# Performance work log

Measured on AMD Instinct MI355X. Metric: run time of the kernel, lower is better.

## Reference

```python
import jax, jax.numpy as jnp
import numpy as np

NUM_HEADS = 16
ROPE_BASE = 10000.0


def _rotate_half(x):
    d = x.shape[-1] // 2
    return jnp.concatenate([-x[..., d:], x[..., :d]], axis=-1)


def _rope_cos_sin(seq_len, rot_dim, dtype):
    # LlamaRotaryEmbedding(dim=rot_dim): inv_freq over even indices, emb = cat(freqs, freqs)
    inv_freq = 1.0 / (ROPE_BASE ** (jnp.arange(0, rot_dim, 2, dtype=jnp.float32) / rot_dim))
    t = jnp.arange(seq_len, dtype=jnp.float32)
    freqs = t[:, None] * inv_freq[None, :]            # [S, rot_dim/2]
    emb = jnp.concatenate([freqs, freqs], axis=-1)    # [S, rot_dim]
    return jnp.cos(emb).astype(dtype), jnp.sin(emb).astype(dtype)


def setup_inputs() -> dict:
    key = jax.random.key(0)
    ks = jax.random.split(key, 9)
    B, S, H = 2, 2048, 2048
    L = H // 8
    s = 0.02
    return {
        "hidden_states": jax.random.normal(ks[0], (B, S, H), jnp.float32),
        "Wkv_d": jax.random.normal(ks[1], (H, L), jnp.float32) * s,
        "Wq_d": jax.random.normal(ks[2], (H, L), jnp.float32) * s,
        "Wk_u": jax.random.normal(ks[3], (L, H // 2), jnp.float32) * s,
        "Wq_u": jax.random.normal(ks[4], (L, H // 2), jnp.float32) * s,
        "Wv_u": jax.random.normal(ks[5], (L, H), jnp.float32) * s,
        "Wrk": jax.random.normal(ks[6], (H, H // 2), jnp.float32) * s,
        "Wrq": jax.random.normal(ks[7], (L, H // 2), jnp.float32) * s,
        "Wo": jax.random.normal(ks[8], (H, H), jnp.float32) * s,
    }


def reference(hidden_states, Wkv_d, Wq_d, Wk_u, Wq_u, Wv_u, Wrk, Wrq, Wo):
    B, S, H = hidden_states.shape
    nh = NUM_HEADS
    hd = H // nh          # 128
    rd = hd // 2          # 64 (rope / content half width)

    kv_d = hidden_states @ Wkv_d            # [B,S,L]
    q_d = hidden_states @ Wq_d              # [B,S,L]

    k_c = (kv_d @ Wk_u).reshape(B, S, nh, rd)
    q_c = (q_d @ Wq_u).reshape(B, S, nh, rd)
    v = (kv_d @ Wv_u).reshape(B, S, nh, hd)
    k_r = (hidden_states @ Wrk).reshape(B, S, nh, rd)
    q_r = (q_d @ Wrq).reshape(B, S, nh, rd)

    cos, sin = _rope_cos_sin(S, rd, hidden_states.dtype)
    cos = cos[None, :, None, :]             # [1,S,1,rd] broadcast over batch/heads
    sin = sin[None, :, None, :]
    q_r = q_r * cos + _rotate_half(q_r) * sin
    k_r = k_r * cos + _rotate_half(k_r) * sin

    q = jnp.concatenate([q_c, q_r], axis=-1).transpose(0, 2, 1, 3)  # [B,nh,S,hd]
    k = jnp.concatenate([k_c, k_r], axis=-1).transpose(0, 2, 1, 3)
    v = v.transpose(0, 2, 1, 3)

    scale = jnp.asarray(hd, q.dtype) ** -0.5
    scores = jnp.einsum("bhqd,bhkd->bhqk", q, k) * scale
    causal = jnp.tril(jnp.ones((S, S), dtype=bool))
    scores = jnp.where(causal[None, None], scores, jnp.finfo(scores.dtype).min)
    attn = jax.nn.softmax(scores, axis=-1)
    y = jnp.einsum("bhqk,bhkd->bhqd", attn, v)
    y = y.transpose(0, 2, 1, 3).reshape(B, S, H)
    return y @ Wo
```

## Files before the change

### kernel.cpp

```cpp
#include <hip/hip_runtime.h>
#include <hip/hip_bf16.h>
#include <math.h>


typedef __attribute__((ext_vector_type(8))) short bf16x8;
typedef __attribute__((ext_vector_type(4))) float f32x4;
typedef unsigned int u32;

#define MFMA16(a, b, c) __builtin_amdgcn_mfma_f32_16x16x32_bf16(a, b, c, 0, 0, 0)

#define QSCALE_F (0.08838834764831845f * 1.4426950408889634f)
#define ROPE_EXP (-0.2878231366242557f)

__device__ __forceinline__ short f2bs(float f) {
  __hip_bfloat16 h = __float2bfloat16(f);
  return *reinterpret_cast<short*>(&h);
}
__device__ __forceinline__ float bs2f(short s) {
  union { unsigned int u; float f; } v;
  v.u = ((unsigned int)(unsigned short)s) << 16;
  return v.f;
}
__device__ __forceinline__ u32 fbits(float f) {
  union { float f; u32 u; } v; v.f = f; return v.u;
}

__device__ __forceinline__ void async16(const void* g, void* l) {
  __builtin_amdgcn_global_load_lds(
      (const __attribute__((address_space(1))) u32*)(unsigned long long)g,
      (__attribute__((address_space(3))) u32*)(unsigned int)(unsigned long long)l,
      16, 0, 0);
}
__device__ __forceinline__ void wait_vm0() {
  __builtin_amdgcn_s_waitcnt(0x0f70);
}

__device__ __forceinline__ void xcd_remap(int& bx, int& by) {
  const int id = blockIdx.y * gridDim.x + blockIdx.x;
  const int nyp = gridDim.y >> 3;
  const int xcd = id & 7, t = id >> 3;
  by = xcd * nyp + (t % nyp);
  bx = t / nyp;
}

__device__ __forceinline__ void wtrans_tile(const float* __restrict__ W,
                                            short* __restrict__ Wt, int K, int N,
                                            int bx, int by, int tid) {
  __shared__ float t[32][33];
  int k0 = by * 32, n0 = bx * 32;
#pragma unroll
  for (int i = 0; i < 4; ++i) {
    int idx = tid + i * 256;
    int r = idx >> 5, c = idx & 31;
    t[r][c] = W[(size_t)(k0 + r) * N + n0 + c];
  }
  __syncthreads();
#pragma unroll
  for (int i = 0; i < 4; ++i) {
    int idx = tid + i * 256;
    int r = idx >> 5, c = idx & 31;
    Wt[(size_t)(n0 + r) * K + k0 + c] = f2bs(t[c][r]);
  }
}

__global__ __launch_bounds__(256) void prep_all(
    const float* __restrict__ hs, const float* __restrict__ Wkvd,
    const float* __restrict__ Wqd, const float* __restrict__ Wku,
    const float* __restrict__ Wqu, const float* __restrict__ Wvu,
    const float* __restrict__ Wrk, const float* __restrict__ Wrq,
    const float* __restrict__ Wo, short* __restrict__ hs_b,
    short* __restrict__ W1t, short* __restrict__ W2t,
    short* __restrict__ W3t, short* __restrict__ Wo_t) {
  const int b = blockIdx.x, tid = threadIdx.x;
  if (b < 8192) {
    int i = (b * 256 + tid) * 4;
    float4 v = *(const float4*)(hs + i);
    short4 o;
    o.x = f2bs(v.x); o.y = f2bs(v.y); o.z = f2bs(v.z); o.w = f2bs(v.w);
    *(short4*)(hs_b + i) = o;
  } else if (b < 8704) {
    int l = b - 8192; wtrans_tile(Wkvd, W1t, 2048, 256, l & 7, l >> 3, tid);
  } else if (b < 9216) {
    int l = b - 8704; wtrans_tile(Wqd, W1t + 256 * 2048, 2048, 256, l & 7, l >> 3, tid);
  } else if (b < 11264) {
    int l = b - 9216; wtrans_tile(Wrk, W1t + 512 * 2048, 2048, 1024, l & 31, l >> 5, tid);
  } else if (b < 11520) {
    int l = b - 11264; wtrans_tile(Wku, W2t, 256, 1024, l & 31, l >> 5, tid);
  } else if (b < 12032) {
    int l = b - 11520; wtrans_tile(Wvu, W2t + 1024 * 256, 256, 2048, l & 63, l >> 6, tid);
  } else if (b < 12288) {
    int l = b - 12032; wtrans_tile(Wqu, W3t, 256, 1024, l & 31, l >> 5, tid);
  } else if (b < 12544) {
    int l = b - 12288; wtrans_tile(Wrq, W3t + 1024 * 256, 256, 1024, l & 31, l >> 5, tid);
  } else {
    int l = b - 12544; wtrans_tile(Wo, Wo_t, 2048, 2048, l & 63, l >> 6, tid);
  }
}

__device__ __forceinline__ void cstore(float v, float* p) { *p = v; }
__device__ __forceinline__ void cstore(float v, short* p) { *p = f2bs(v); }

template <typename CT>
__global__ __launch_bounds__(256) void gemm_bt(const short* __restrict__ A, int lda,
                                               const short* __restrict__ Bt, int ldb,
                                               CT* __restrict__ C, int ldc, int K) {
  __shared__ short As[128 * 64];
  __shared__ short Bs[128 * 64];
  const int tid = threadIdx.x;
  const int wave = tid >> 6, lane = tid & 63;
  const int quad = lane >> 4, l15 = lane & 15;
  const int wm = wave & 1, wn = wave >> 1;
  int bx, by; xcd_remap(bx, by);
  const int row0 = by * 128, col0 = bx * 128;
  const int sr = tid >> 3;
  const int sc = ((tid & 7) ^ (sr & 7)) * 8;
  const short* Ag = A + (size_t)(row0 + sr) * lda + sc;
  const short* Bg = Bt + (size_t)(col0 + sr) * ldb + sc;
  const int rk = l15 & 7;

  f32x4 acc[4][4];
#pragma unroll
  for (int i = 0; i < 4; ++i)
#pragma unroll
    for (int j = 0; j < 4; ++j) acc[i][j] = {0.f, 0.f, 0.f, 0.f};

  for (int k0 = 0; k0 < K; k0 += 64) {
    __syncthreads();
#pragma unroll
    for (int i = 0; i < 4; ++i) {
      async16(Ag + (size_t)(i * 32) * lda + k0, &As[i * 2048 + tid * 8]);
      async16(Bg + (size_t)(i * 32) * ldb + k0, &Bs[i * 2048 + tid * 8]);
    }
    wait_vm0();
    __syncthreads();
#pragma unroll
    for (int s = 0; s < 2; ++s) {
      bf16x8 af[4], bfr[4];
#pragma unroll
      for (int i = 0; i < 4; ++i) {
        af[i]  = *(const bf16x8*)&As[(wm * 64 + i * 16 + l15) * 64 +
                                     ((s * 4 + quad) ^ rk) * 8];
        bfr[i] = *(const bf16x8*)&Bs[(wn * 64 + i * 16 + l15) * 64 +
                                     ((s * 4 + quad) ^ rk) * 8];
      }
#pragma unroll
      for (int i = 0; i < 4; ++i)
#pragma unroll
        for (int j = 0; j < 4; ++j)
          acc[i][j] = MFMA16(af[i], bfr[j], acc[i][j]);
    }
  }
#pragma unroll
  for (int i = 0; i < 4; ++i)
#pragma unroll
    for (int j = 0; j < 4; ++j)
#pragma unroll
      for (int r = 0; r < 4; ++r) {
        int row = row0 + wm * 64 + i * 16 + quad * 4 + r;
        int col = col0 + wn * 64 + j * 16 + l15;
        cstore(acc[i][j][r], &C[(size_t)row * ldc + col]);
      }
}

__global__ __launch_bounds__(256) void gemm1k(const short* __restrict__ A,
                                              const short* __restrict__ Bt,
                                              short* __restrict__ C1,
                                              short* __restrict__ kf) {
  __shared__ short As[128 * 64];
  __shared__ short Bs[128 * 64];
  const int tid = threadIdx.x;
  const int wave = tid >> 6, lane = tid & 63;
  const int quad = lane >> 4, l15 = lane & 15;
  const int wm = wave & 1, wn = wave >> 1;
  int bx, by; xcd_remap(bx, by);
  const int row0 = by * 128, col0 = bx * 128;
  const int sr = tid >> 3;
  const int sc = ((tid & 7) ^ (sr & 7)) * 8;
  const short* Ag = A + (size_t)(row0 + sr) * 2048 + sc;
  const short* Bg = Bt + (size_t)(col0 + sr) * 2048 + sc;
  const int rk = l15 & 7;

  f32x4 acc[4][4];
#pragma unroll
  for (int i = 0; i < 4; ++i)
#pragma unroll
    for (int j = 0; j < 4; ++j) acc[i][j] = {0.f, 0.f, 0.f, 0.f};

  for (int k0 = 0; k0 < 2048; k0 += 64) {
    __syncthreads();
#pragma unroll
    for (int i = 0; i < 4; ++i) {
      async16(Ag + (size_t)(i * 32) * 2048 + k0, &As[i * 2048 + tid * 8]);
      async16(Bg + (size_t)(i * 32) * 2048 + k0, &Bs[i * 2048 + tid * 8]);
    }
    wait_vm0();
    __syncthreads();
#pragma unroll
    for (int s = 0; s < 2; ++s) {
      bf16x8 af[4], bfr[4];
#pragma unroll
      for (int i = 0; i < 4; ++i) {
        af[i]  = *(const bf16x8*)&As[(wm * 64 + i * 16 + l15) * 64 +
                                     ((s * 4 + quad) ^ rk) * 8];
        bfr[i] = *(const bf16x8*)&Bs[(wn * 64 + i * 16 + l15) * 64 +
                                     ((s * 4 + quad) ^ rk) * 8];
      }
#pragma unroll
      for (int i = 0; i < 4; ++i)
#pragma unroll
        for (int j = 0; j < 4; ++j)
          acc[i][j] = MFMA16(af[i], bfr[j], acc[i][j]);
    }
  }

  if (bx < 4) {
#pragma unroll
    for (int i = 0; i < 4; ++i)
#pragma unroll
      for (int jj = 0; jj < 4; ++jj)
#pragma unroll
        for (int r = 0; r < 4; ++r) {
          int row = row0 + wm * 64 + i * 16 + quad * 4 + r;
          int col = col0 + wn * 64 + jj * 16 + l15;
          C1[(size_t)row * 512 + col] = f2bs(acc[i][jj][r]);
        }
  } else {
    const int colb = (bx - 4) * 128 + wn * 64 + l15;
    const int h = colb >> 6;
    const float ef0 = __expf(ROPE_EXP * (float)l15);
    const float ef1 = __expf(ROPE_EXP * (float)(l15 + 16));
#pragma unroll
    for (int i = 0; i < 4; ++i)
#pragma unroll
      for (int r = 0; r < 4; ++r) {
        int row = row0 + wm * 64 + i * 16 + quad * 4 + r;
        int s = row & 2047, b = row >> 11;
        float fs = (float)s;
        float a0 = fs * ef0, a1 = fs * ef1;
        float c0 = __cosf(a0), s0 = __sinf(a0);
        float c1 = __cosf(a1), s1 = __sinf(a1);
        float o0 = acc[i][0][r] * c0 - acc[i][2][r] * s0;
        float o2 = acc[i][2][r] * c0 + acc[i][0][r] * s0;
        float o1 = acc[i][1][r] * c1 - acc[i][3][r] * s1;
        float o3 = acc[i][3][r] * c1 + acc[i][1][r] * s1;
        short* kp = kf + (((size_t)(b * 16 + h) * 2048 + s) * 128 + 64 + l15);
        kp[0]  = f2bs(o0);
        kp[16] = f2bs(o1);
        kp[32] = f2bs(o2);
        kp[48] = f2bs(o3);
      }
  }
}

__global__ __launch_bounds__(256) void gemm23(const short* __restrict__ C1,
                                              const short* __restrict__ W2t,
                                              short* __restrict__ qf,
                                              short* __restrict__ kf,
                                              short* __restrict__ vt) {
  __shared__ short As[128 * 64];
  __shared__ short Bs[128 * 64];
  const int tid = threadIdx.x;
  const int wave = tid >> 6, lane = tid & 63;
  const int quad = lane >> 4, l15 = lane & 15;
  const int wm = wave & 1, wn = wave >> 1;
  int bx, by; xcd_remap(bx, by);
  const short* A = bx < 24 ? C1 : C1 + 256;
  const int row0 = by * 128;
  const int sr = tid >> 3;
  const int sc = ((tid & 7) ^ (sr & 7)) * 8;
  const short* Ag = A + (size_t)(row0 + sr) * 512 + sc;
  const short* Bg = W2t + (size_t)(bx * 128 + sr) * 256 + sc;
  const int rk = l15 & 7;

  f32x4 acc[4][4];
#pragma unroll
  for (int i = 0; i < 4; ++i)
#pragma unroll
    for (int j = 0; j < 4; ++j) acc[i][j] = {0.f, 0.f, 0.f, 0.f};

  for (int k0 = 0; k0 < 256; k0 += 64) {
    __syncthreads();
#pragma unroll
    for (int i = 0; i < 4; ++i) {
      async16(Ag + (size_t)(i * 32) * 512 + k0, &As[i * 2048 + tid * 8]);
      async16(Bg + (size_t)(i * 32) * 256 + k0, &Bs[i * 2048 + tid * 8]);
    }
    wait_vm0();
    __syncthreads();
#pragma unroll
    for (int s = 0; s < 2; ++s) {
      bf16x8 af[4], bfr[4];
#pragma unroll
      for (int i = 0; i < 4; ++i) {
        af[i]  = *(const bf16x8*)&As[(wm * 64 + i * 16 + l15) * 64 +
                                     ((s * 4 + quad) ^ rk) * 8];
        bfr[i] = *(const bf16x8*)&Bs[(wn * 64 + i * 16 + l15) * 64 +
                                     ((s * 4 + quad) ^ rk) * 8];
      }
#pragma unroll
      for (int i = 0; i < 4; ++i)
#pragma unroll
        for (int j = 0; j < 4; ++j)
          acc[i][j] = MFMA16(af[i], bfr[j], acc[i][j]);
    }
  }

  if (bx < 8) {
    const int colb = bx * 128 + wn * 64 + l15;
    const int h = colb >> 6;
#pragma unroll
    for (int i = 0; i < 4; ++i)
#pragma unroll
      for (int r = 0; r < 4; ++r) {
        int row = row0 + wm * 64 + i * 16 + quad * 4 + r;
        int s = row & 2047, b = row >> 11;
        short* kp = kf + (((size_t)(b * 16 + h) * 2048 + s) * 128 + l15);
#pragma unroll
        for (int jj = 0; jj < 4; ++jj) kp[jj * 16] = f2bs(acc[i][jj][r]);
      }
  } else if (bx < 24) {
    const int b = row0 >> 11;
    const int s0 = row0 & 2047;
#pragma unroll
    for (int i = 0; i < 4; ++i)
#pragma unroll
      for (int jj = 0; jj < 4; ++jj) {
        int vcol = (bx - 8) * 128 + wn * 64 + jj * 16 + l15;
        int h = vcol >> 7, d = vcol & 127;
        int s = s0 + wm * 64 + i * 16 + quad * 4;
        short4 o;
        o.x = f2bs(acc[i][jj][0]); o.y = f2bs(acc[i][jj][1]);
        o.z = f2bs(acc[i][jj][2]); o.w = f2bs(acc[i][jj][3]);
        *(short4*)&vt[((size_t)((b * 16 + h) * 128 + d)) * 2048 + s] = o;
      }
  } else if (bx < 32) {
    const int colb = (bx - 24) * 128 + wn * 64 + l15;
    const int h = colb >> 6;
#pragma unroll
    for (int i = 0; i < 4; ++i)
#pragma unroll
      for (int r = 0; r < 4; ++r) {
        int row = row0 + wm * 64 + i * 16 + quad * 4 + r;
        int s = row & 2047, b = row >> 11;
        short* qp = qf + (((size_t)(b * 16 + h) * 2048 + s) * 128 + l15);
#pragma unroll
        for (int jj = 0; jj < 4; ++jj) qp[jj * 16] = f2bs(acc[i][jj][r] * QSCALE_F);
      }
  } else {
    const int colb = (bx - 32) * 128 + wn * 64 + l15;
    const int h = colb >> 6;
    const float ef0 = __expf(ROPE_EXP * (float)l15);
    const float ef1 = __expf(ROPE_EXP * (float)(l15 + 16));
#pragma unroll
    for (int i = 0; i < 4; ++i)
#pragma unroll
      for (int r = 0; r < 4; ++r) {
        int row = row0 + wm * 64 + i * 16 + quad * 4 + r;
        int s = row & 2047, b = row >> 11;
        float fs = (float)s;
        float a0 = fs * ef0, a1 = fs * ef1;
        float c0 = __cosf(a0), s0 = __sinf(a0);
        float c1 = __cosf(a1), s1 = __sinf(a1);
        float o0 = (acc[i][0][r] * c0 - acc[i][2][r] * s0) * QSCALE_F;
        float o2 = (acc[i][2][r] * c0 + acc[i][0][r] * s0) * QSCALE_F;
        float o1 = (acc[i][1][r] * c1 - acc[i][3][r] * s1) * QSCALE_F;
        float o3 = (acc[i][3][r] * c1 + acc[i][1][r] * s1) * QSCALE_F;
        short* qp = qf + (((size_t)(b * 16 + h) * 2048 + s) * 128 + 64 + l15);
        qp[0]  = f2bs(o0);
        qp[16] = f2bs(o1);
        qp[32] = f2bs(o2);
        qp[48] = f2bs(o3);
      }
  }
}

__global__ __launch_bounds__(256) void attn_split(const short* __restrict__ qf,
                                                  const short* __restrict__ kf,
                                                  const short* __restrict__ vt,
                                                  short* __restrict__ part,
                                                  float2* __restrict__ ml) {
  __shared__ short Ks[2][32 * 128];
  __shared__ short Vs[2][128 * 32];
  __shared__ short Pw[4][16 * 32];
  const int lid = blockIdx.x;
  const int bh = (lid & 7) * 4 + ((lid >> 3) & 3);
  const int x  = lid >> 5;
  const int tid = threadIdx.x;
  const int wave = tid >> 6, lane = tid & 63;
  const int quad = lane >> 4, l15 = lane & 15;
  const int krow_l = tid >> 4;
  const int kcol_sw = ((tid & 15) ^ krow_l) * 8;
  const int vrow_l = tid >> 2;
  const int vcol_sw = ((tid & 3) ^ (vrow_l & 3) ^ ((vrow_l >> 2) & 3)) * 8;
  const short* kgB = kf + (((size_t)bh * 2048) + krow_l) * 128 + kcol_sw;
  const short* vgB = vt + ((size_t)bh * 128 + vrow_l) * 2048 + vcol_sw;
  const int pswz = l15 & 6;

  for (int pass = 0; pass < 2; ++pass) {
    const int qt = pass ? 31 - x : x;
    const int ks = pass ? qt + 1 : 0;
    const int ke = pass ? 2 * (qt + 1) : x + 1;
    const int q0w = qt * 64 + wave * 16;

    bf16x8 qfr[4];
    {
      const short* qp = qf + (((size_t)bh * 2048) + q0w + l15) * 128;
#pragma unroll
      for (int kc = 0; kc < 4; ++kc)
        qfr[kc] = *(const bf16x8*)(qp + kc * 32 + quad * 8);
    }
    float m_i = -INFINITY;
    float l_i = 0.f;
    f32x4 O[8];
#pragma unroll
    for (int dt = 0; dt < 8; ++dt) O[dt] = {0.f, 0.f, 0.f, 0.f};

    {
      const short* kg = kgB + (size_t)ks * 32 * 128;
      const short* vg = vgB + ks * 32;
#pragma unroll
      for (int i = 0; i < 2; ++i) {
        async16(kg + (size_t)i * 16 * 128, &Ks[0][i * 2048 + tid * 8]);
        async16(vg + (size_t)i * 64 * 2048, &Vs[0][i * 2048 + tid * 8]);
      }
    }
    wait_vm0();
    __syncthreads();

    int cur = 0;
    for (int kt = ks; kt < ke; ++kt) {
      const int k0 = kt * 32;
      if (kt + 1 < ke) {
        const short* kg = kgB + (size_t)(kt + 1) * 32 * 128;
        const short* vg = vgB + (kt + 1) * 32;
#pragma unroll
        for (int i = 0; i < 2; ++i) {
          async16(kg + (size_t)i * 16 * 128, &Ks[cur ^ 1][i * 2048 + tid * 8]);
          async16(vg + (size_t)i * 64 * 2048, &Vs[cur ^ 1][i * 2048 + tid * 8]);
        }
      }

      f32x4 St[2];
#pragma unroll
      for (int j = 0; j < 2; ++j) St[j] = {0.f, 0.f, 0.f, 0.f};
      __builtin_amdgcn_s_setprio(1);
#pragma unroll
      for (int kc = 0; kc < 4; ++kc) {
        bf16x8 kb[2];
#pragma unroll
        for (int j = 0; j < 2; ++j)
          kb[j] = *(const bf16x8*)&Ks[cur][(j * 16 + l15) * 128 +
                                          (((kc * 4 + quad) ^ l15) & 15) * 8];
#pragma unroll
        for (int j = 0; j < 2; ++j)
          St[j] = MFMA16(kb[j], qfr[kc], St[j]);
      }
      __builtin_amdgcn_s_setprio(0);

      if (kt >= 2 * qt) {
#pragma unroll
        for (int j = 0; j < 2; ++j)
#pragma unroll
          for (int r = 0; r < 4; ++r)
            if (k0 + j * 16 + quad * 4 + r > q0w + l15)
              St[j][r] = -INFINITY;
      }

      {
        float mt = -INFINITY;
#pragma unroll
        for (int j = 0; j < 2; ++j)
#pragma unroll
          for (int r = 0; r < 4; ++r) mt = fmaxf(mt, St[j][r]);
        if (!__all(mt <= m_i + 8.f)) {
          mt = fmaxf(mt, __shfl_xor(mt, 16));
          mt = fmaxf(mt, __shfl_xor(mt, 32));
          float mnew = fmaxf(m_i, mt);
          float a = __builtin_amdgcn_exp2f(m_i - mnew);
          m_i = mnew;
          l_i *= a;
#pragma unroll
          for (int dt = 0; dt < 8; ++dt)
#pragma unroll
            for (int r = 0; r < 4; ++r) O[dt][r] *= a;
        }
        float ms = (m_i == -INFINITY) ? 0.f : m_i;
        float ps = 0.f;
#pragma unroll
        for (int j = 0; j < 2; ++j)
#pragma unroll
          for (int r = 0; r < 4; ++r) {
            float p = __builtin_amdgcn_exp2f(St[j][r] - ms);
            St[j][r] = p;
            ps += p;
          }
        l_i += ps;
      }

      {
        int pr = l15;
#pragma unroll
        for (int j = 0; j < 2; ++j) {
          u32 u0 = (fbits(St[j][1]) & 0xffff0000u) | (fbits(St[j][0]) >> 16);
          u32 u1 = (fbits(St[j][3]) & 0xffff0000u) | (fbits(St[j][2]) >> 16);
          uint2 pk; pk.x = u0; pk.y = u1;
          int g = (j * 4 + quad) ^ pswz;
          *(uint2*)&Pw[wave][pr * 32 + g * 4] = pk;
        }
      }

      __builtin_amdgcn_s_setprio(1);
      bf16x8 pa;
      {
        int g = (quad * 2) ^ pswz;
        pa = *(const bf16x8*)&Pw[wave][l15 * 32 + g * 4];
      }
#pragma unroll
      for (int dt = 0; dt < 8; ++dt) {
        bf16x8 vb = *(const bf16x8*)&Vs[cur][(dt * 16 + l15) * 32 +
                                            ((quad ^ (l15 & 3) ^ ((l15 >> 2) & 3)) & 3) * 8];
        O[dt] = MFMA16(vb, pa, O[dt]);
      }
      __builtin_amdgcn_s_setprio(0);

      wait_vm0();
      __syncthreads();
      cur ^= 1;
    }

    const int pidx = (bh * 32 + qt) * 2 + pass;
    short* pb = part + (size_t)pidx * 64 * 128;
    {
      int qrow = wave * 16 + l15;
#pragma unroll
      for (int dt = 0; dt < 8; ++dt) {
        short4 o;
        o.x = f2bs(O[dt][0]); o.y = f2bs(O[dt][1]);
        o.z = f2bs(O[dt][2]); o.w = f2bs(O[dt][3]);
        *(short4*)&pb[(size_t)qrow * 128 + dt * 16 + quad * 4] = o;
      }
    }
    float lr = l_i;
    lr += __shfl_xor(lr, 16);
    lr += __shfl_xor(lr, 32);
    if (quad == 0) {
      float2 v; v.x = m_i; v.y = lr;
      ml[pidx * 64 + wave * 16 + l15] = v;
    }
  }
}

__global__ __launch_bounds__(256) void attn_merge(const short* __restrict__ part,
                                                  const float2* __restrict__ ml,
                                                  short* __restrict__ y) {
  const int l = blockIdx.x;
  const int bh = ((l & 7) << 2) | ((l >> 3) & 3);
  const int qt = (l >> 5) & 31;
  const int b = bh >> 4, h = bh & 15;
  const int row = threadIdx.x >> 2, d0 = (threadIdx.x & 3) * 32;
  const int p1 = (bh * 32 + qt) * 2, p2 = p1 + 1;
  float2 a = ml[p1 * 64 + row], c = ml[p2 * 64 + row];
  float m = fmaxf(a.x, c.x);
  float a1 = __builtin_amdgcn_exp2f(a.x - m);
  float a2 = __builtin_amdgcn_exp2f(c.x - m);
  float invl = 1.f / (a.y * a1 + c.y * a2);
  a1 *= invl; a2 *= invl;
  const short* s1 = part + ((size_t)p1 * 64 + row) * 128 + d0;
  const short* s2 = part + ((size_t)p2 * 64 + row) * 128 + d0;
  short* yp = y + (((size_t)b * 2048 + qt * 64 + row) * 16 + h) * 128 + d0;
#pragma unroll
  for (int j = 0; j < 8; ++j) {
    short4 v1 = *(const short4*)(s1 + j * 4);
    short4 v2 = *(const short4*)(s2 + j * 4);
    short4 o;
    o.x = f2bs(bs2f(v1.x) * a1 + bs2f(v2.x) * a2);
    o.y = f2bs(bs2f(v1.y) * a1 + bs2f(v2.y) * a2);
    o.z = f2bs(bs2f(v1.z) * a1 + bs2f(v2.z) * a2);
    o.w = f2bs(bs2f(v1.w) * a1 + bs2f(v2.w) * a2);
    *(short4*)(yp + j * 4) = o;
  }
}

extern "C" void kernel_launch(void* const* d_in, const int* in_sizes, int n_in,
                              void* d_out, int out_size, void* d_ws, size_t ws_size,
                              hipStream_t stream) {
  const float* hs   = (const float*)d_in[0];
  const float* Wkvd = (const float*)d_in[1];
  const float* Wqd  = (const float*)d_in[2];
  const float* Wku  = (const float*)d_in[3];
  const float* Wqu  = (const float*)d_in[4];
  const float* Wvu  = (const float*)d_in[5];
  const float* Wrk  = (const float*)d_in[6];
  const float* Wrq  = (const float*)d_in[7];
  const float* Wo   = (const float*)d_in[8];
  float* out = (float*)d_out;
  char* ws = (char*)d_ws;
  const size_t MB = 1024ull * 1024ull;

  short* hs_b = (short*)(ws + 0 * MB);
  short* W1t  = (short*)(ws + 16 * MB);
  short* W2t  = (short*)(ws + 22 * MB);
  short* W3t  = W2t + 3072 * 256;
  short* C1   = (short*)(ws + 25 * MB);
  short* Wo_t = (short*)(ws + 77 * MB);
  short* q_f  = (short*)(ws + 85 * MB);
  short* k_f  = (short*)(ws + 101 * MB);
  short* v_t  = (short*)(ws + 117 * MB);
  short* y_b  = (short*)(ws + 133 * MB);
  short*  partb = (short*)(ws + 0 * MB);
  float2* mlb   = (float2*)(ws + 32 * MB);

  dim3 blk(256);
  prep_all<<<dim3(16640), blk, 0, stream>>>(hs, Wkvd, Wqd, Wku, Wqu, Wvu, Wrk,
                                            Wrq, Wo, hs_b, W1t, W2t, W3t, Wo_t);

  gemm1k<<<dim3(12, 32), blk, 0, stream>>>(hs_b, W1t, C1, k_f);
  gemm23<<<dim3(40, 32), blk, 0, stream>>>(C1, W2t, q_f, k_f, v_t);

  attn_split<<<dim3(1024), blk, 0, stream>>>(q_f, k_f, v_t, partb, mlb);
  attn_merge<<<dim3(1024), blk, 0, stream>>>(partb, mlb, y_b);

  gemm_bt<float><<<dim3(16, 32), blk, 0, stream>>>(y_b, 2048, Wo_t, 2048, out, 2048, 2048);
}
```

Measured before the change: 315.3 us.

## Double-buffer LDS tiles in GEMM kernels to overlap loads with MFMA

Converts the three projection GEMM kernels from single-buffered to double-buffered shared memory. The next K-tile is prefetched asynchronously while MFMAs run on the current one, and wave priority is raised during the compute phase. The goal is to hide global-load latency that the old load-wait-compute loop exposed every iteration. LDS use per block doubles to 64KB, which may lower occupancy.

Measured after the change: 289.4 us, median of 2. -8.2%, faster.

```diff
diff --git a/kernel.cpp b/kernel.cpp
--- a/kernel.cpp
+++ b/kernel.cpp
@@ -104,8 +104,8 @@
 __global__ __launch_bounds__(256) void gemm_bt(const short* __restrict__ A, int lda,
                                                const short* __restrict__ Bt, int ldb,
                                                CT* __restrict__ C, int ldc, int K) {
-  __shared__ short As[128 * 64];
-  __shared__ short Bs[128 * 64];
+  __shared__ short As[2][128 * 64];
+  __shared__ short Bs[2][128 * 64];
   const int tid = threadIdx.x;
   const int wave = tid >> 6, lane = tid & 63;
   const int quad = lane >> 4, l15 = lane & 15;
@@ -124,31 +124,44 @@
 #pragma unroll
     for (int j = 0; j < 4; ++j) acc[i][j] = {0.f, 0.f, 0.f, 0.f};
 
+#pragma unroll
+  for (int i = 0; i < 4; ++i) {
+    async16(Ag + (size_t)(i * 32) * lda, &As[0][i * 2048 + tid * 8]);
+    async16(Bg + (size_t)(i * 32) * ldb, &Bs[0][i * 2048 + tid * 8]);
+  }
+  wait_vm0();
+  __syncthreads();
+
+  int cur = 0;
   for (int k0 = 0; k0 < K; k0 += 64) {
-    __syncthreads();
-#pragma unroll
-    for (int i = 0; i < 4; ++i) {
-      async16(Ag + (size_t)(i * 32) * lda + k0, &As[i * 2048 + tid * 8]);
-      async16(Bg + (size_t)(i * 32) * ldb + k0, &Bs[i * 2048 + tid * 8]);
-    }
+    if (k0 + 64 < K) {
+#pragma unroll
+      for (int i = 0; i < 4; ++i) {
+        async16(Ag + (size_t)(i * 32) * lda + k0 + 64, &As[cur ^ 1][i * 2048 + tid * 8]);
+        async16(Bg + (size_t)(i * 32) * ldb + k0 + 64, &Bs[cur ^ 1][i * 2048 + tid * 8]);
+      }
+    }
+    __builtin_amdgcn_s_setprio(1);
+#pragma unroll
+    for (int s = 0; s < 2; ++s) {
+      bf16x8 af[4], bfr[4];
+#pragma unroll
+      for (int i = 0; i < 4; ++i) {
+        af[i]  = *(const bf16x8*)&As[cur][(wm * 64 + i * 16 + l15) * 64 +
+                                         ((s * 4 + quad) ^ rk) * 8];
+        bfr[i] = *(const bf16x8*)&Bs[cur][(wn * 64 + i * 16 + l15) * 64 +
+                                         ((s * 4 + quad) ^ rk) * 8];
+      }
+#pragma unroll
+      for (int i = 0; i < 4; ++i)
+#pragma unroll
+        for (int j = 0; j < 4; ++j)
+          acc[i][j] = MFMA16(af[i], bfr[j], acc[i][j]);
+    }
+    __builtin_amdgcn_s_setprio(0);
     wait_vm0();
     __syncthreads();
-#pragma unroll
-    for (int s = 0; s < 2; ++s) {
-      bf16x8 af[4], bfr[4];
-#pragma unroll
-      for (int i = 0; i < 4; ++i) {
-        af[i]  = *(const bf16x8*)&As[(wm * 64 + i * 16 + l15) * 64 +
-                                     ((s * 4 + quad) ^ rk) * 8];
-        bfr[i] = *(const bf16x8*)&Bs[(wn * 64 + i * 16 + l15) * 64 +
-                                     ((s * 4 + quad) ^ rk) * 8];
-      }
-#pragma unroll
-      for (int i = 0; i < 4; ++i)
-#pragma unroll
-        for (int j = 0; j < 4; ++j)
-          acc[i][j] = MFMA16(af[i], bfr[j], acc[i][j]);
-    }
+    cur ^= 1;
   }
 #pragma unroll
   for (int i = 0; i < 4; ++i)
@@ -166,8 +179,8 @@
                                               const short* __restrict__ Bt,
                                               short* __restrict__ C1,
                                               short* __restrict__ kf) {
-  __shared__ short As[128 * 64];
-  __shared__ short Bs[128 * 64];
+  __shared__ short As[2][128 * 64];
+  __shared__ short Bs[2][128 * 64];
   const int tid = threadIdx.x;
   const int wave = tid >> 6, lane = tid & 63;
   const int quad = lane >> 4, l15 = lane & 15;
@@ -186,31 +199,44 @@
 #pragma unroll
     for (int j = 0; j < 4; ++j) acc[i][j] = {0.f, 0.f, 0.f, 0.f};
 
+#pragma unroll
+  for (int i = 0; i < 4; ++i) {
+    async16(Ag + (size_t)(i * 32) * 2048, &As[0][i * 2048 + tid * 8]);
+    async16(Bg + (size_t)(i * 32) * 2048, &Bs[0][i * 2048 + tid * 8]);
+  }
+  wait_vm0();
+  __syncthreads();
+
+  int cur = 0;
   for (int k0 = 0; k0 < 2048; k0 += 64) {
-    __syncthreads();
-#pragma unroll
-    for (int i = 0; i < 4; ++i) {
-      async16(Ag + (size_t)(i * 32) * 2048 + k0, &As[i * 2048 + tid * 8]);
-      async16(Bg + (size_t)(i * 32) * 2048 + k0, &Bs[i * 2048 + tid * 8]);
-    }
+    if (k0 + 64 < 2048) {
+#pragma unroll
+      for (int i = 0; i < 4; ++i) {
+        async16(Ag + (size_t)(i * 32) * 2048 + k0 + 64, &As[cur ^ 1][i * 2048 + tid * 8]);
+        async16(Bg + (size_t)(i * 32) * 2048 + k0 + 64, &Bs[cur ^ 1][i * 2048 + tid * 8]);
+      }
+    }
+    __builtin_amdgcn_s_setprio(1);
+#pragma unroll
+    for (int s = 0; s < 2; ++s) {
+      bf16x8 af[4], bfr[4];
+#pragma unroll
+      for (int i = 0; i < 4; ++i) {
+        af[i]  = *(const bf16x8*)&As[cur][(wm * 64 + i * 16 + l15) * 64 +
+                                         ((s * 4 + quad) ^ rk) * 8];
+        bfr[i] = *(const bf16x8*)&Bs[cur][(wn * 64 + i * 16 + l15) * 64 +
+                                         ((s * 4 + quad) ^ rk) * 8];
+      }
+#pragma unroll
+      for (int i = 0; i < 4; ++i)
+#pragma unroll
+        for (int j = 0; j < 4; ++j)
+          acc[i][j] = MFMA16(af[i], bfr[j], acc[i][j]);
+    }
+    __builtin_amdgcn_s_setprio(0);
     wait_vm0();
     __syncthreads();
-#pragma unroll
-    for (int s = 0; s < 2; ++s) {
-      bf16x8 af[4], bfr[4];
-#pragma unroll
-      for (int i = 0; i < 4; ++i) {
-        af[i]  = *(const bf16x8*)&As[(wm * 64 + i * 16 + l15) * 64 +
-                                     ((s * 4 + quad) ^ rk) * 8];
-        bfr[i] = *(const bf16x8*)&Bs[(wn * 64 + i * 16 + l15) * 64 +
-                                     ((s * 4 + quad) ^ rk) * 8];
-      }
-#pragma unroll
-      for (int i = 0; i < 4; ++i)
-#pragma unroll
-        for (int j = 0; j < 4; ++j)
-          acc[i][j] = MFMA16(af[i], bfr[j], acc[i][j]);
-    }
+    cur ^= 1;
   }
 
   if (bx < 4) {
@@ -257,8 +283,8 @@
                                               short* __restrict__ qf,
                                               short* __restrict__ kf,
                                               short* __restrict__ vt) {
-  __shared__ short As[128 * 64];
-  __shared__ short Bs[128 * 64];
+  __shared__ short As[2][128 * 64];
+  __shared__ short Bs[2][128 * 64];
   const int tid = threadIdx.x;
   const int wave = tid >> 6, lane = tid & 63;
   const int quad = lane >> 4, l15 = lane & 15;
@@ -278,31 +304,44 @@
 #pragma unroll
     for (int j = 0; j < 4; ++j) acc[i][j] = {0.f, 0.f, 0.f, 0.f};
 
+#pragma unroll
+  for (int i = 0; i < 4; ++i) {
+    async16(Ag + (size_t)(i * 32) * 512, &As[0][i * 2048 + tid * 8]);
+    async16(Bg + (size_t)(i * 32) * 256, &Bs[0][i * 2048 + tid * 8]);
+  }
+  wait_vm0();
+  __syncthreads();
+
+  int cur = 0;
   for (int k0 = 0; k0 < 256; k0 += 64) {
-    __syncthreads();
-#pragma unroll
-    for (int i = 0; i < 4; ++i) {
-      async16(Ag + (size_t)(i * 32) * 512 + k0, &As[i * 2048 + tid * 8]);
-      async16(Bg + (size_t)(i * 32) * 256 + k0, &Bs[i * 2048 + tid * 8]);
-    }
+    if (k0 + 64 < 256) {
+#pragma unroll
+      for (int i = 0; i < 4; ++i) {
+        async16(Ag + (size_t)(i * 32) * 512 + k0 + 64, &As[cur ^ 1][i * 2048 + tid * 8]);
+        async16(Bg + (size_t)(i * 32) * 256 + k0 + 64, &Bs[cur ^ 1][i * 2048 + tid * 8]);
+      }
+    }
+    __builtin_amdgcn_s_setprio(1);
+#pragma unroll
+    for (int s = 0; s < 2; ++s) {
+      bf16x8 af[4], bfr[4];
+#pragma unroll
+      for (int i = 0; i < 4; ++i) {
+        af[i]  = *(const bf16x8*)&As[cur][(wm * 64 + i * 16 + l15) * 64 +
+                                         ((s * 4 + quad) ^ rk) * 8];
+        bfr[i] = *(const bf16x8*)&Bs[cur][(wn * 64 + i * 16 + l15) * 64 +
+                                         ((s * 4 + quad) ^ rk) * 8];
+      }
+#pragma unroll
+      for (int i = 0; i < 4; ++i)
+#pragma unroll
+        for (int j = 0; j < 4; ++j)
+          acc[i][j] = MFMA16(af[i], bfr[j], acc[i][j]);
+    }
+    __builtin_amdgcn_s_setprio(0);
     wait_vm0();
     __syncthreads();
-#pragma unroll
-    for (int s = 0; s < 2; ++s) {
-      bf16x8 af[4], bfr[4];
-#pragma unroll
-      for (int i = 0; i < 4; ++i) {
-        af[i]  = *(const bf16x8*)&As[(wm * 64 + i * 16 + l15) * 64 +
-                                     ((s * 4 + quad) ^ rk) * 8];
-        bfr[i] = *(const bf16x8*)&Bs[(wn * 64 + i * 16 + l15) * 64 +
-                                     ((s * 4 + quad) ^ rk) * 8];
-      }
-#pragma unroll
-      for (int i = 0; i < 4; ++i)
-#pragma unroll
-        for (int j = 0; j < 4; ++j)
-          acc[i][j] = MFMA16(af[i], bfr[j], acc[i][j]);
-    }
+    cur ^= 1;
   }
 
   if (bx < 8) {
```
